# Performance work log

Hardware: AMD Instinct MI355X
Metric: run time of the kernel (lower is better)

Reference implementation:

```python
import jax, jax.numpy as jnp
import numpy as np

EPS = 1e-6
N = 512
D = 8192


def solve_lap_np(cost):
    """Jonker-Volgenant shortest-augmenting-path LAP (same optimum as
    scipy.optimize.linear_sum_assignment). Returns col4row: col assigned to each row."""
    cost = np.asarray(cost, dtype=np.float64)
    n = cost.shape[0]
    u = np.zeros(n)
    v = np.zeros(n)
    path = np.full(n, -1, dtype=np.int64)
    col4row = np.full(n, -1, dtype=np.int64)
    row4col = np.full(n, -1, dtype=np.int64)
    for cur_row in range(n):
        shortest = np.full(n, np.inf)
        SR = np.zeros(n, dtype=bool)  # visited rows
        SC = np.zeros(n, dtype=bool)  # visited cols
        i = cur_row
        min_val = 0.0
        sink = -1
        while sink == -1:
            SR[i] = True
            idx = np.nonzero(~SC)[0]
            r = min_val + cost[i, idx] - u[i] - v[idx]
            upd = r < shortest[idx]
            shortest[idx[upd]] = r[upd]
            path[idx[upd]] = i
            j = idx[np.argmin(shortest[idx])]
            min_val = shortest[j]
            SC[j] = True
            if row4col[j] == -1:
                sink = j
            else:
                i = row4col[j]
        # dual updates
        u[cur_row] += min_val
        sr = np.nonzero(SR)[0]
        sr = sr[sr != cur_row]
        u[sr] += min_val - shortest[col4row[sr]]
        sc = np.nonzero(SC)[0]
        v[sc] -= min_val - shortest[sc]
        # augment along the alternating path
        j = sink
        while True:
            i = path[j]
            row4col[j] = i
            col4row[i], j = j, col4row[i]
            if i == cur_row:
                break
    return col4row


def lap_assign(cost):
    """Optimal assignment as a one-hot labelling matrix (rows -> cols)."""
    n = cost.shape[0]
    col = jax.pure_callback(
        lambda c: solve_lap_np(np.asarray(c)).astype(np.int32),
        jax.ShapeDtypeStruct((n,), jnp.int32),
        cost,
    )
    return jax.nn.one_hot(col, n, dtype=cost.dtype)


def l2_normalize(x):
    # torch F.normalize(p=2, dim=1): x / max(||x||, eps)
    norm = jnp.sqrt(jnp.sum(x * x, axis=1, keepdims=True))
    return x / jnp.maximum(norm, EPS)


def setup_inputs() -> dict:
    key = jax.random.key(0)
    k1, k2, k3 = jax.random.split(key, 3)
    return {
        "un1": jax.random.normal(k1, (N, D), dtype=jnp.float32),
        "un2": jax.random.normal(k2, (N, D), dtype=jnp.float32),
        "un3": jax.random.normal(k3, (N, D), dtype=jnp.float32),
    }


def reference(un1, un2, un3):
    n1 = l2_normalize(un1)
    n2 = l2_normalize(un2)
    n3 = l2_normalize(un3)
    # cosine-distance cost matrices, cycle 1->2->3->1
    c12 = 1.0 - n1 @ n2.T
    c23 = 1.0 - n2 @ n3.T
    c31 = 1.0 - n3 @ n1.T
    x12 = lap_assign(c12)
    x23 = lap_assign(c23)
    x31 = lap_assign(c31)
    return (x12, x23, x31)
```

## Files before the change

### kernel.cpp

```cpp
#include <hip/hip_runtime.h>
#include <math.h>

#define NN 512
#define DD 8192

__global__ __launch_bounds__(256) void norm_kernel(
    const float* __restrict__ a0, const float* __restrict__ a1,
    const float* __restrict__ a2, float* __restrict__ scales) {
  const float* mats[3] = {a0, a1, a2};
  const int m = blockIdx.y;
  const int row = blockIdx.x;
  const float* x = mats[m] + (size_t)row * DD;
  const int tid = threadIdx.x;
  float s = 0.f;
  for (int k = tid * 4; k < DD; k += 256 * 4) {
    const float4 v = *(const float4*)(x + k);
    s += v.x * v.x + v.y * v.y + v.z * v.z + v.w * v.w;
  }
#pragma unroll
  for (int off = 32; off > 0; off >>= 1) s += __shfl_down(s, off);
  __shared__ float ws[4];
  if ((tid & 63) == 0) ws[tid >> 6] = s;
  __syncthreads();
  if (tid == 0) {
    const float t = ws[0] + ws[1] + ws[2] + ws[3];
    scales[m * NN + row] = 1.0f / fmaxf(sqrtf(t), 1e-6f);
  }
}

__global__ __launch_bounds__(256) void cost_gemm_kernel(
    const float* __restrict__ a0, const float* __restrict__ a1,
    const float* __restrict__ a2, const float* __restrict__ scales,
    float* __restrict__ cost_all) {
  const float* mats[3] = {a0, a1, a2};
  const int p = blockIdx.z;
  const int pA = p, pB = (p + 1) % 3;
  const float* A = mats[pA];
  const float* B = mats[pB];
  float* C = cost_all + (size_t)p * NN * NN;

  __shared__ float lds_a[32 * 64];
  __shared__ float lds_b[32 * 64];

  const int tid = threadIdx.x;
  const int rowBase = blockIdx.y * 64;
  const int colBase = blockIdx.x * 64;

  const int lr = tid & 63;
  const int lq = tid >> 6;

  const float* Arow = A + (size_t)(rowBase + lr) * DD;
  const float* Brow = B + (size_t)(colBase + lr) * DD;

  float acc[4][4];
#pragma unroll
  for (int i = 0; i < 4; ++i)
#pragma unroll
    for (int j = 0; j < 4; ++j) acc[i][j] = 0.f;

  const int tx = tid & 15, ty = tid >> 4;

  for (int kb = 0; kb < DD; kb += 32) {
#pragma unroll
    for (int qq = 0; qq < 2; ++qq) {
      const int q = lq + qq * 4;
      const float4 av = *(const float4*)(Arow + kb + q * 4);
      const float4 bv = *(const float4*)(Brow + kb + q * 4);
      lds_a[(q * 4 + 0) * 64 + lr] = av.x;
      lds_a[(q * 4 + 1) * 64 + lr] = av.y;
      lds_a[(q * 4 + 2) * 64 + lr] = av.z;
      lds_a[(q * 4 + 3) * 64 + lr] = av.w;
      lds_b[(q * 4 + 0) * 64 + lr] = bv.x;
      lds_b[(q * 4 + 1) * 64 + lr] = bv.y;
      lds_b[(q * 4 + 2) * 64 + lr] = bv.z;
      lds_b[(q * 4 + 3) * 64 + lr] = bv.w;
    }
    __syncthreads();
#pragma unroll
    for (int k = 0; k < 32; ++k) {
      const float4 a4 = *(const float4*)(&lds_a[k * 64 + ty * 4]);
      const float4 b4 = *(const float4*)(&lds_b[k * 64 + tx * 4]);
      const float as0[4] = {a4.x, a4.y, a4.z, a4.w};
      const float bs0[4] = {b4.x, b4.y, b4.z, b4.w};
#pragma unroll
      for (int ii = 0; ii < 4; ++ii)
#pragma unroll
        for (int jj = 0; jj < 4; ++jj)
          acc[ii][jj] = fmaf(as0[ii], bs0[jj], acc[ii][jj]);
    }
    __syncthreads();
  }

#pragma unroll
  for (int ii = 0; ii < 4; ++ii) {
    const int gr = rowBase + ty * 4 + ii;
    const float sa = scales[pA * NN + gr];
#pragma unroll
    for (int jj = 0; jj < 4; ++jj) {
      const int gc = colBase + tx * 4 + jj;
      const float sb = scales[pB * NN + gc];
      C[gr * NN + gc] = 1.0f - acc[ii][jj] * sa * sb;
    }
  }
}


__device__ __forceinline__ int SW(int c) { return ((c & 7) << 6) | (c >> 3); }

__device__ __forceinline__ unsigned wave_min_u32(unsigned x) {
  int t;
  t = __builtin_amdgcn_update_dpp((int)x, (int)x, 0x111, 0xf, 0xf, false);
  x = ((unsigned)t < x) ? (unsigned)t : x;
  t = __builtin_amdgcn_update_dpp((int)x, (int)x, 0x112, 0xf, 0xf, false);
  x = ((unsigned)t < x) ? (unsigned)t : x;
  t = __builtin_amdgcn_update_dpp((int)x, (int)x, 0x114, 0xf, 0xf, false);
  x = ((unsigned)t < x) ? (unsigned)t : x;
  t = __builtin_amdgcn_update_dpp((int)x, (int)x, 0x118, 0xf, 0xf, false);
  x = ((unsigned)t < x) ? (unsigned)t : x;
  t = __builtin_amdgcn_update_dpp((int)x, (int)x, 0x142, 0xf, 0xf, false);
  x = ((unsigned)t < x) ? (unsigned)t : x;
  t = __builtin_amdgcn_update_dpp((int)x, (int)x, 0x143, 0xf, 0xf, false);
  x = ((unsigned)t < x) ? (unsigned)t : x;
  return (unsigned)__builtin_amdgcn_readlane((int)x, 63);
}

__device__ __forceinline__ double readlane_f64(double x, int lane) {
  const long long b = __double_as_longlong(x);
  const int lo = __builtin_amdgcn_readlane((int)(b & 0xffffffffLL), lane);
  const int hi = __builtin_amdgcn_readlane((int)(b >> 32), lane);
  return __longlong_as_double(((long long)hi << 32) | (unsigned long long)(unsigned)lo);
}

__global__ __launch_bounds__(64) void lap_kernel(
    const float* __restrict__ cost_all, float* __restrict__ out) {
  const int p = blockIdx.x;
  const float* cost = cost_all + (size_t)p * NN * NN;
  float* outp = out + (size_t)p * NN * NN;
  const int tid = threadIdx.x;

  __shared__ double sh_u[NN];
  __shared__ double sh_shortest[NN];
  __shared__ int sh_path[NN];
  __shared__ int sh_col4row[NN];
  __shared__ int sh_row4col[NN];

  const double INF = __builtin_inf();

  for (int k = tid; k < NN; k += 64) {
    sh_u[k] = 0.0;
    sh_col4row[k] = -1;
    sh_row4col[k] = -1;
  }
  double myV[8];
#pragma unroll
  for (int q = 0; q < 8; ++q) myV[q] = 0.0;
  __syncthreads();

  for (int cur_row = 0; cur_row < NN; ++cur_row) {
    double selv[8];
    double vAdj[8];
    double frz[8];
    int myPath[8];
    unsigned pl[8];
#pragma unroll
    for (int q = 0; q < 8; ++q) {
      selv[q] = INF;
      vAdj[q] = myV[q];
      frz[q] = 0.0;
      myPath[q] = 0;
    }
#pragma unroll
    for (int q = 0; q < 8; ++q)
      pl[q] = ((unsigned)q << 10) | (unsigned)(sh_row4col[SW(tid * 8 + q)] + 1);

    unsigned scMask = 0, srMask = 0;
    int i = cur_row;
    double minv = 0.0;
    int sink = -1;
    int pendQ = -1, pendLane = 0;

    while (true) {
      if ((i >> 3) == tid) srMask |= 1u << (i & 7);
      const float4 c0 = *(const float4*)(cost + (size_t)i * NN + tid * 8);
      const float4 c1 = *(const float4*)(cost + (size_t)i * NN + tid * 8 + 4);
      const double u_i = sh_u[SW(i)];
      if (pendQ >= 0) {
        const bool me = (tid == pendLane);
#define APPLY_SC(K)                                                     \
        if (pendQ == K) {                                               \
          if (me) {                                                     \
            selv[K] = INF; vAdj[K] = -INF; frz[K] = minv;               \
            scMask |= 1u << K;                                          \
          }                                                             \
        }
        APPLY_SC(0) APPLY_SC(1) APPLY_SC(2) APPLY_SC(3)
        APPLY_SC(4) APPLY_SC(5) APPLY_SC(6) APPLY_SC(7)
#undef APPLY_SC
      }
      const float cf[8] = {c0.x, c0.y, c0.z, c0.w, c1.x, c1.y, c1.z, c1.w};
#pragma unroll
      for (int q = 0; q < 8; ++q) {
        const double r = ((minv + (double)cf[q]) - u_i) - vAdj[q];
        const bool cnd = r < selv[q];
        selv[q] = fmin(selv[q], r);
        myPath[q] = cnd ? i : myPath[q];
      }
      const bool t01 = selv[1] < selv[0];
      double v01 = t01 ? selv[1] : selv[0]; unsigned p01 = t01 ? pl[1] : pl[0];
      const bool t23 = selv[3] < selv[2];
      double v23 = t23 ? selv[3] : selv[2]; unsigned p23 = t23 ? pl[3] : pl[2];
      const bool t45 = selv[5] < selv[4];
      double v45 = t45 ? selv[5] : selv[4]; unsigned p45 = t45 ? pl[5] : pl[4];
      const bool t67 = selv[7] < selv[6];
      double v67 = t67 ? selv[7] : selv[6]; unsigned p67 = t67 ? pl[7] : pl[6];
      const bool ta = v23 < v01;
      const double vab = ta ? v23 : v01; const unsigned pab = ta ? p23 : p01;
      const bool tb = v67 < v45;
      const double vcd = tb ? v67 : v45; const unsigned pcd = tb ? p67 : p45;
      const bool tc = vcd < vab;
      const double lv = tc ? vcd : vab; const unsigned lp = tc ? pcd : pab;
      const long long bb = __double_as_longlong(lv);
      const unsigned long long kk =
          (bb < 0) ? ~(unsigned long long)bb
                   : ((unsigned long long)bb | 0x8000000000000000ULL);
      const unsigned hi = (unsigned)(kk >> 32);
      const unsigned lo = (unsigned)kk;
      const unsigned minhi = wave_min_u32(hi);
      unsigned long long bal = __ballot(hi == minhi);
      int srcLane;
      if (__popcll(bal) == 1) {
        srcLane = __ffsll(bal) - 1;
      } else {
        const unsigned lo2 = (hi == minhi) ? lo : 0xFFFFFFFFu;
        const unsigned minlo = wave_min_u32(lo2);
        bal = __ballot((hi == minhi) && (lo == minlo));
        srcLane = __ffsll(bal) - 1;
      }
      minv = readlane_f64(lv, srcLane);
      const unsigned pw = (unsigned)__builtin_amdgcn_readlane((int)lp, srcLane);
      const int qb = (int)(pw >> 10);
      const int r4 = (int)(pw & 0x3FFu) - 1;
      if (r4 < 0) {
        sink = srcLane * 8 + qb;
        break;
      }
      i = r4;
      pendQ = qb;
      pendLane = srcLane;
    }

#pragma unroll
    for (int q = 0; q < 8; ++q) {
      sh_shortest[SW(tid * 8 + q)] = frz[q];
      sh_path[SW(tid * 8 + q)] = myPath[q];
    }
    __syncthreads();
#pragma unroll
    for (int q = 0; q < 8; ++q) {
      const int row = tid * 8 + q;
      if (row == cur_row) {
        sh_u[SW(row)] += minv;
      } else if (srMask & (1u << q)) {
        sh_u[SW(row)] += minv - sh_shortest[SW(sh_col4row[SW(row)])];
      }
      if (scMask & (1u << q)) myV[q] -= minv - frz[q];
    }
    __syncthreads();
    if (tid == 0) {
      int j = sink;
      while (true) {
        const int pi = sh_path[SW(j)];
        sh_row4col[SW(j)] = pi;
        const int tmp = sh_col4row[SW(pi)];
        sh_col4row[SW(pi)] = j;
        j = tmp;
        if (pi == cur_row) break;
      }
    }
    __syncthreads();
  }

#pragma unroll
  for (int q = 0; q < 8; ++q) {
    const int row = tid * 8 + q;
    outp[(size_t)row * NN + sh_col4row[SW(row)]] = 1.0f;
  }
}

extern "C" void kernel_launch(void* const* d_in, const int* in_sizes, int n_in,
                              void* d_out, int out_size, void* d_ws, size_t ws_size,
                              hipStream_t stream) {
  const float* un1 = (const float*)d_in[0];
  const float* un2 = (const float*)d_in[1];
  const float* un3 = (const float*)d_in[2];
  float* out = (float*)d_out;

  float* cost = (float*)d_ws;
  float* scales = cost + (size_t)3 * NN * NN;

  hipMemsetAsync(d_out, 0, (size_t)out_size * sizeof(float), stream);

  norm_kernel<<<dim3(NN, 3), 256, 0, stream>>>(un1, un2, un3, scales);
  cost_gemm_kernel<<<dim3(NN / 64, NN / 64, 3), 256, 0, stream>>>(un1, un2, un3, scales, cost);
  lap_kernel<<<3, 64, 0, stream>>>(cost, out);
}
```

Before: 5.735 ms.

## Deepen GEMM K-tile and hoist loop-invariant terms in LAP relaxation

The cost GEMM now stages 64-wide K tiles in LDS instead of 32, halving the number of barriers per tile, with a partial unroll of the inner loop. In the LAP inner loop, minv - u_i - vAdj is precomputed per element so each relaxation is a single add. A few statements are also reordered and arrays renamed. The rounding change in the relaxation could alter tie-breaking relative to the reference ordering of operations.

```diff
diff --git a/kernel.cpp b/kernel.cpp
--- a/kernel.cpp
+++ b/kernel.cpp
@@ -39,8 +39,8 @@
   const float* B = mats[pB];
   float* C = cost_all + (size_t)p * NN * NN;
 
-  __shared__ float lds_a[32 * 64];
-  __shared__ float lds_b[32 * 64];
+  __shared__ float lds_a[64 * 64];
+  __shared__ float lds_b[64 * 64];
 
   const int tid = threadIdx.x;
   const int rowBase = blockIdx.y * 64;
@@ -60,9 +60,9 @@
 
   const int tx = tid & 15, ty = tid >> 4;
 
-  for (int kb = 0; kb < DD; kb += 32) {
-#pragma unroll
-    for (int qq = 0; qq < 2; ++qq) {
+  for (int kb = 0; kb < DD; kb += 64) {
+#pragma unroll
+    for (int qq = 0; qq < 4; ++qq) {
       const int q = lq + qq * 4;
       const float4 av = *(const float4*)(Arow + kb + q * 4);
       const float4 bv = *(const float4*)(Brow + kb + q * 4);
@@ -76,8 +76,8 @@
       lds_b[(q * 4 + 3) * 64 + lr] = bv.w;
     }
     __syncthreads();
-#pragma unroll
-    for (int k = 0; k < 32; ++k) {
+#pragma unroll 8
+    for (int k = 0; k < 64; ++k) {
       const float4 a4 = *(const float4*)(&lds_a[k * 64 + ty * 4]);
       const float4 b4 = *(const float4*)(&lds_b[k * 64 + tx * 4]);
       const float as0[4] = {a4.x, a4.y, a4.z, a4.w};
@@ -129,6 +129,12 @@
   const int lo = __builtin_amdgcn_readlane((int)(b & 0xffffffffLL), lane);
   const int hi = __builtin_amdgcn_readlane((int)(b >> 32), lane);
   return __longlong_as_double(((long long)hi << 32) | (unsigned long long)(unsigned)lo);
+}
+
+__device__ __forceinline__ unsigned long long f64key(double x) {
+  const long long b = __double_as_longlong(x);
+  return (b < 0) ? ~(unsigned long long)b
+                 : ((unsigned long long)b | 0x8000000000000000ULL);
 }
 
 __global__ __launch_bounds__(64) void lap_kernel(
@@ -141,15 +147,17 @@
   __shared__ double sh_u[NN];
   __shared__ double sh_shortest[NN];
   __shared__ int sh_path[NN];
-  __shared__ int sh_col4row[NN];
-  __shared__ int sh_row4col[NN];
+  __shared__ int sh_x[NN];
+  __shared__ int sh_y[NN];
 
   const double INF = __builtin_inf();
 
-  for (int k = tid; k < NN; k += 64) {
-    sh_u[k] = 0.0;
-    sh_col4row[k] = -1;
-    sh_row4col[k] = -1;
+#pragma unroll
+  for (int q = 0; q < 8; ++q) {
+    const int e = tid * 8 + q;
+    sh_x[SW(e)] = -1;
+    sh_y[SW(e)] = -1;
+    sh_u[SW(e)] = 0.0;
   }
   double myV[8];
 #pragma unroll
@@ -171,7 +179,7 @@
     }
 #pragma unroll
     for (int q = 0; q < 8; ++q)
-      pl[q] = ((unsigned)q << 10) | (unsigned)(sh_row4col[SW(tid * 8 + q)] + 1);
+      pl[q] = ((unsigned)q << 10) | (unsigned)(sh_y[SW(tid * 8 + q)] + 1);
 
     unsigned scMask = 0, srMask = 0;
     int i = cur_row;
@@ -180,10 +188,10 @@
     int pendQ = -1, pendLane = 0;
 
     while (true) {
-      if ((i >> 3) == tid) srMask |= 1u << (i & 7);
       const float4 c0 = *(const float4*)(cost + (size_t)i * NN + tid * 8);
       const float4 c1 = *(const float4*)(cost + (size_t)i * NN + tid * 8 + 4);
       const double u_i = sh_u[SW(i)];
+      if ((i >> 3) == tid) srMask |= 1u << (i & 7);
       if (pendQ >= 0) {
         const bool me = (tid == pendLane);
 #define APPLY_SC(K)                                                     \
@@ -197,10 +205,14 @@
         APPLY_SC(4) APPLY_SC(5) APPLY_SC(6) APPLY_SC(7)
 #undef APPLY_SC
       }
+      const double mu = minv - u_i;
+      double base[8];
+#pragma unroll
+      for (int q = 0; q < 8; ++q) base[q] = mu - vAdj[q];
       const float cf[8] = {c0.x, c0.y, c0.z, c0.w, c1.x, c1.y, c1.z, c1.w};
 #pragma unroll
       for (int q = 0; q < 8; ++q) {
-        const double r = ((minv + (double)cf[q]) - u_i) - vAdj[q];
+        const double r = (double)cf[q] + base[q];
         const bool cnd = r < selv[q];
         selv[q] = fmin(selv[q], r);
         myPath[q] = cnd ? i : myPath[q];
@@ -219,10 +231,7 @@
       const double vcd = tb ? v67 : v45; const unsigned pcd = tb ? p67 : p45;
       const bool tc = vcd < vab;
       const double lv = tc ? vcd : vab; const unsigned lp = tc ? pcd : pab;
-      const long long bb = __double_as_longlong(lv);
-      const unsigned long long kk =
-          (bb < 0) ? ~(unsigned long long)bb
-                   : ((unsigned long long)bb | 0x8000000000000000ULL);
+      const unsigned long long kk = f64key(lv);
       const unsigned hi = (unsigned)(kk >> 32);
       const unsigned lo = (unsigned)kk;
       const unsigned minhi = wave_min_u32(hi);
@@ -236,10 +245,10 @@
         bal = __ballot((hi == minhi) && (lo == minlo));
         srcLane = __ffsll(bal) - 1;
       }
-      minv = readlane_f64(lv, srcLane);
       const unsigned pw = (unsigned)__builtin_amdgcn_readlane((int)lp, srcLane);
       const int qb = (int)(pw >> 10);
       const int r4 = (int)(pw & 0x3FFu) - 1;
+      minv = readlane_f64(lv, srcLane);
       if (r4 < 0) {
         sink = srcLane * 8 + qb;
         break;
@@ -261,7 +270,7 @@
       if (row == cur_row) {
         sh_u[SW(row)] += minv;
       } else if (srMask & (1u << q)) {
-        sh_u[SW(row)] += minv - sh_shortest[SW(sh_col4row[SW(row)])];
+        sh_u[SW(row)] += minv - sh_shortest[SW(sh_x[SW(row)])];
       }
       if (scMask & (1u << q)) myV[q] -= minv - frz[q];
     }
@@ -270,9 +279,9 @@
       int j = sink;
       while (true) {
         const int pi = sh_path[SW(j)];
-        sh_row4col[SW(j)] = pi;
-        const int tmp = sh_col4row[SW(pi)];
-        sh_col4row[SW(pi)] = j;
+        sh_y[SW(j)] = pi;
+        const int tmp = sh_x[SW(pi)];
+        sh_x[SW(pi)] = j;
         j = tmp;
         if (pi == cur_row) break;
       }
@@ -283,7 +292,7 @@
 #pragma unroll
   for (int q = 0; q < 8; ++q) {
     const int row = tid * 8 + q;
-    outp[(size_t)row * NN + sh_col4row[SW(row)]] = 1.0f;
+    outp[(size_t)row * NN + sh_x[SW(row)]] = 1.0f;
   }
 }
 
```

New measurement: 5.883 ms. 2.6% more time.
